# Kernel optimization log

Hardware: AMD Instinct MI355X
Metric: run time of the kernel (lower is better)

## Reference

```python
import jax, jax.numpy as jnp
import numpy as np

B, S, H = 2, 2048, 1024
NH, HD = 16, 64
EPS = 1e-12
SCALE = float(np.sqrt(HD))


def layer_norm(x, g, b, eps=EPS):
    m = jnp.mean(x, axis=-1, keepdims=True)
    v = jnp.mean(jnp.square(x - m), axis=-1, keepdims=True)
    return (x - m) * jax.lax.rsqrt(v + eps) * g + b


def setup_inputs() -> dict:
    key = jax.random.key(0)
    ks = jax.random.split(key, 12)
    std = 0.02 / np.sqrt(2 * 24)  # num_hidden_layers = 24
    return {
        "hidden_states": jax.random.normal(ks[0], (B, S, H), dtype=jnp.float32),
        "attention_mask": jnp.ones((B, S), dtype=jnp.float32),
        "Wq": jax.random.normal(ks[1], (H, H), dtype=jnp.float32) * std,
        "bq": jnp.zeros((H,), dtype=jnp.float32),
        "Wk": jax.random.normal(ks[2], (H, H), dtype=jnp.float32) * std,
        "bk": jnp.zeros((H,), dtype=jnp.float32),
        "Wv": jax.random.normal(ks[3], (H, H), dtype=jnp.float32) * std,
        "bv": jnp.zeros((H,), dtype=jnp.float32),
        "Wd": jax.random.normal(ks[4], (H, H), dtype=jnp.float32) * (1.0 / np.sqrt(H)),
        "bd": jnp.zeros((H,), dtype=jnp.float32),
        "ln_g": jnp.ones((H,), dtype=jnp.float32),
        "ln_b": jnp.zeros((H,), dtype=jnp.float32),
    }


def reference(hidden_states, attention_mask, Wq, bq, Wk, bk, Wv, bv, Wd, bd, ln_g, ln_b):
    x = hidden_states
    # NOTE: source computes pre_attention_norm(x) but the no-cache path uses raw x for Q/K/V.
    def heads(t):  # [B,S,H] -> [B,NH,S,HD]
        return t.reshape(B, S, NH, HD).transpose(0, 2, 1, 3)

    q = heads(x @ Wq.T + bq)
    k = heads(x @ Wk.T + bk)
    v = heads(x @ Wv.T + bv)

    scores = jnp.einsum("bhqd,bhkd->bhqk", q, k) / SCALE
    mask = (1.0 - attention_mask) * -10000.0  # [B,S] -> broadcast [B,1,1,S]
    scores = scores + mask[:, None, None, :]
    probs = jax.nn.softmax(scores.astype(jnp.float32), axis=-1).astype(x.dtype)

    ctx = jnp.einsum("bhqk,bhkd->bhqd", probs, v)
    ctx = ctx.transpose(0, 2, 1, 3).reshape(B, S, NH * HD)

    out = ctx @ Wd.T + bd
    out = layer_norm(out + x, ln_g, ln_b)
    out = jnp.where(jnp.isfinite(out), out, jnp.zeros_like(out))
    return out
```

## Files before the change

kernel.cpp:

```cpp
#include <hip/hip_runtime.h>
#include <cstdint>
#include <cstddef>

#define B_    2
#define S_    2048
#define H_    1024
#define NH_   16
#define HD_   64

typedef __attribute__((ext_vector_type(8)))  __bf16 bf16x8;
typedef __attribute__((ext_vector_type(4)))  __bf16 bf16x4;
typedef __attribute__((ext_vector_type(4)))  float  f32x4;
typedef __attribute__((ext_vector_type(16))) float  f32x16;
typedef __attribute__((ext_vector_type(4)))  unsigned u32x4;

typedef __attribute__((address_space(1))) const unsigned int gcu32_t;
typedef __attribute__((address_space(3))) unsigned int lu32_t;
#define GLOAD16(gp, lp) __builtin_amdgcn_global_load_lds((gcu32_t*)(gp), (lu32_t*)(lp), 16, 0, 0)

#if __has_builtin(__builtin_amdgcn_exp2f)
#define EXP2F(x) __builtin_amdgcn_exp2f(x)
#else
#define EXP2F(x) exp2f(x)
#endif

#define SC_Q 0.1803368977f

__device__ __forceinline__ short f2bf(float f) {
  union { float f; unsigned u; } v; v.f = f;
  unsigned r = v.u + 0x7fffu + ((v.u >> 16) & 1u);
  return (short)(r >> 16);
}

__global__ __launch_bounds__(256) void convert_kernel(
    const float* __restrict__ x,  const float* __restrict__ wq,
    const float* __restrict__ wk, const float* __restrict__ wv,
    const float* __restrict__ wd,
    short* __restrict__ xb,  short* __restrict__ wqb, short* __restrict__ wkb,
    short* __restrict__ wvb, short* __restrict__ wdb) {
  size_t i = ((size_t)blockIdx.x * 256 + threadIdx.x) * 4;
  const float* src; short* dst; size_t off;
  if      (i < 4194304u) { src = x;  dst = xb;  off = i; }
  else if (i < 5242880u) { src = wq; dst = wqb; off = i - 4194304u; }
  else if (i < 6291456u) { src = wk; dst = wkb; off = i - 5242880u; }
  else if (i < 7340032u) { src = wv; dst = wvb; off = i - 6291456u; }
  else                   { src = wd; dst = wdb; off = i - 7340032u; }
  float4 v = *(const float4*)(src + off);
  short4 o; o.x = f2bf(v.x); o.y = f2bf(v.y); o.z = f2bf(v.z); o.w = f2bf(v.w);
  *(short4*)(dst + off) = o;
}

template<int MODE>
__global__ __launch_bounds__(256, 3) void gemm_bt(
    const short* __restrict__ A,
    const short* __restrict__ Bq, const short* __restrict__ Bk,
    const short* __restrict__ Bv,
    const float* __restrict__ biasq, const float* __restrict__ biask,
    const float* __restrict__ biasv,
    short* __restrict__ outq, short* __restrict__ outk, short* __restrict__ outv,
    float* __restrict__ outy) {
  __shared__ short As[128 * 64];
  __shared__ short Bs[128 * 64];

  const short* Bw; const float* bias; short* outs = nullptr;
  float qscale = 1.0f;
  if (MODE == 0) {
    int z = blockIdx.z;
    Bw   = (z == 0) ? Bq    : ((z == 1) ? Bk    : Bv);
    bias = (z == 0) ? biasq : ((z == 1) ? biask : biasv);
    outs = (z == 0) ? outq  : ((z == 1) ? outk  : outv);
    if (z == 0) qscale = SC_Q;
  } else {
    Bw = Bq; bias = biasq;
  }

  const int K = 1024;
  int tid  = threadIdx.x;
  int lane = tid & 63, w = tid >> 6;
  int wr = w >> 1, wc = w & 1;
  int m0 = blockIdx.y * 128, n0 = blockIdx.x * 128;
  int l15 = lane & 15, lg = lane >> 4;

  int lr = lane >> 3, lc8 = 8 * ((lane & 7) ^ lr);
  const short* Ag = A  + (size_t)(m0 + w * 8 + lr) * K + lc8;
  const short* Bg = Bw + (size_t)(n0 + w * 8 + lr) * K + lc8;

  int cxor = (l15 & 7) * 8;

  f32x4 acc[4][4];
  for (int m = 0; m < 4; m++)
    for (int n = 0; n < 4; n++) acc[m][n] = {0.f, 0.f, 0.f, 0.f};

  for (int kt = 0; kt < 16; kt++) {
    __syncthreads();
    for (int it = 0; it < 4; it++) {
      GLOAD16(Ag + (size_t)it * 32 * K + kt * 64, &As[(w * 8 + it * 32) * 64]);
      GLOAD16(Bg + (size_t)it * 32 * K + kt * 64, &Bs[(w * 8 + it * 32) * 64]);
    }
    __syncthreads();
#pragma unroll
    for (int kkh = 0; kkh < 2; kkh++) {
      int col = (kkh * 32 + lg * 8) ^ cxor;
      bf16x8 af[4], bfr[4];
#pragma unroll
      for (int m = 0; m < 4; m++)
        af[m] = *(const bf16x8*)&As[(wr * 64 + m * 16 + l15) * 64 + col];
#pragma unroll
      for (int n = 0; n < 4; n++)
        bfr[n] = *(const bf16x8*)&Bs[(wc * 64 + n * 16 + l15) * 64 + col];
#pragma unroll
      for (int m = 0; m < 4; m++)
#pragma unroll
        for (int n = 0; n < 4; n++)
          acc[m][n] = __builtin_amdgcn_mfma_f32_16x16x32_bf16(af[m], bfr[n], acc[m][n], 0, 0, 0);
    }
  }

  for (int n = 0; n < 4; n++) {
    int col = n0 + wc * 64 + n * 16 + l15;
    float bval = bias[col];
    if (MODE == 0) {
      int h = col >> 6, d = col & 63;
      for (int m = 0; m < 4; m++) {
        int rowb = m0 + wr * 64 + m * 16 + lg * 4;
        for (int j = 0; j < 4; j++) {
          int row = rowb + j;
          int bb = row >> 11, s = row & 2047;
          outs[(((size_t)bb * NH_ + h) * S_ + s) * HD_ + d] = f2bf((acc[m][n][j] + bval) * qscale);
        }
      }
    } else {
      for (int m = 0; m < 4; m++) {
        int rowb = m0 + wr * 64 + m * 16 + lg * 4;
        for (int j = 0; j < 4; j++)
          outy[(size_t)(rowb + j) * 1024 + col] = acc[m][n][j] + bval;
      }
    }
  }
}

__global__ __launch_bounds__(256, 2) void attn_kernel(
    const short* __restrict__ Q, const short* __restrict__ K,
    const short* __restrict__ V, const float* __restrict__ mask,
    short* __restrict__ ctx) {
  __shared__ short Ks[2][64 * 64];
  __shared__ short Vs[2][64 * 64];
  __shared__ unsigned long long mbits[32];

  int b = blockIdx.x;
  int bh = (b & 7) * 4 + ((b >> 3) >> 4);
  int qb = (b >> 3) & 15;
  int bidx = bh >> 4, hh = bh & 15;
  int q0 = qb * 128;
  int tid = threadIdx.x, lane = tid & 63, w = tid >> 6;
  int l31 = lane & 31, lh = lane >> 5, l15 = lane & 15;

  const short* Qg = Q + (size_t)bh * S_ * HD_;
  const short* Kg = K + (size_t)bh * S_ * HD_;
  const short* Vg = V + (size_t)bh * S_ * HD_;

  int lr = lane >> 3, lc8 = 8 * ((lane & 7) ^ lr);
  int kxor = (lane & 7) * 8;

  const short* Qrow = Qg + (size_t)(q0 + w * 32 + l31) * HD_;
  bf16x8 qfrag[4];
#pragma unroll
  for (int ks = 0; ks < 4; ks++)
    qfrag[ks] = *(const bf16x8*)&Qrow[ks * 16 + lh * 8];

  GLOAD16(Kg + (size_t)(w * 8 + lr) * HD_ + lc8, &Ks[0][(w * 8) * 64]);
  GLOAD16(Kg + (size_t)(w * 8 + 32 + lr) * HD_ + lc8, &Ks[0][(w * 8 + 32) * 64]);
  int vrow = tid >> 3, vcol = (tid & 7) * 8;
  int voff = ((vrow >> 2) * 4 + (vcol >> 4)) * 64 + (vrow & 3) * 16 + (vcol & 15);
  *(int4*)&Vs[0][voff]        = *(const int4*)&Vg[(size_t)vrow * HD_ + vcol];
  *(int4*)&Vs[0][voff + 2048] = *(const int4*)&Vg[(size_t)(vrow + 32) * HD_ + vcol];
  if (w == 0) {
#pragma unroll 4
    for (int t = 0; t < 32; t++) {
      unsigned long long bb = __ballot(mask[bidx * S_ + t * 64 + lane] > 0.5f);
      if (lane == 0) mbits[t] = bb;
    }
  }
  __syncthreads();

  float mrun = -1e30f, lrun = 0.f;
  f32x16 oacc[2];
#pragma unroll
  for (int dt = 0; dt < 2; dt++)
#pragma unroll
    for (int j = 0; j < 16; j++) oacc[dt][j] = 0.f;

  unsigned vtrb = (unsigned)(uintptr_t)&Vs[0][0]
                + (unsigned)(l15 * 8 + ((lane >> 4) & 1) * 128 + lh * 1024);

  for (int kt = 0; kt < 32; kt++) {
    int cur = kt & 1;

    int4 vp0, vp1;
    if (kt < 31) {
      const short* Kn = Kg + (size_t)(kt + 1) * 64 * HD_;
      GLOAD16(Kn + (size_t)(w * 8 + lr) * HD_ + lc8, &Ks[cur ^ 1][(w * 8) * 64]);
      GLOAD16(Kn + (size_t)(w * 8 + 32 + lr) * HD_ + lc8, &Ks[cur ^ 1][(w * 8 + 32) * 64]);
      const short* Vn = Vg + (size_t)(kt + 1) * 64 * HD_;
      vp0 = *(const int4*)&Vn[(size_t)vrow * HD_ + vcol];
      vp1 = *(const int4*)&Vn[(size_t)(vrow + 32) * HD_ + vcol];
    }

    f32x16 sc[2];
#pragma unroll
    for (int kb = 0; kb < 2; kb++)
#pragma unroll
      for (int j = 0; j < 16; j++) sc[kb][j] = 0.f;
    __builtin_amdgcn_s_setprio(1);
#pragma unroll
    for (int ks = 0; ks < 4; ks++)
#pragma unroll
      for (int kb = 0; kb < 2; kb++) {
        bf16x8 af = *(const bf16x8*)&Ks[cur][(kb * 32 + l31) * 64 + ((ks * 16 + lh * 8) ^ kxor)];
        sc[kb] = __builtin_amdgcn_mfma_f32_32x32x16_bf16(af, qfrag[ks], sc[kb], 0, 0, 0);
      }
    __builtin_amdgcn_s_setprio(0);

    unsigned long long mb = mbits[kt];
    if (__any(mb != ~0ull)) {
      unsigned long long sh = mb >> (lh * 4);
#pragma unroll
      for (int kb = 0; kb < 2; kb++)
#pragma unroll
        for (int r = 0; r < 16; r++)
          if (!((sh >> (kb * 32 + (r & 3) + 8 * (r >> 2))) & 1)) sc[kb][r] = -1e30f;
    }

    float rmax = sc[0][0];
#pragma unroll
    for (int kb = 0; kb < 2; kb++)
#pragma unroll
      for (int r = 0; r < 16; r++) rmax = fmaxf(rmax, sc[kb][r]);
    {
      float xa = rmax, xb = rmax;
      asm volatile("v_permlane32_swap_b32 %0, %1" : "+v"(xa), "+v"(xb));
      rmax = fmaxf(xa, xb);
    }

    if (__any(rmax > mrun + 8.f)) {
      float mn = fmaxf(mrun, rmax);
      float a = EXP2F(mrun - mn);
      lrun *= a; mrun = mn;
#pragma unroll
      for (int dt = 0; dt < 2; dt++)
#pragma unroll
        for (int j = 0; j < 16; j++) oacc[dt][j] *= a;
    }

    float rs_ = 0.f;
#pragma unroll
    for (int kb = 0; kb < 2; kb++)
#pragma unroll
      for (int r = 0; r < 16; r++) {
        float p = EXP2F(sc[kb][r] - mrun);
        sc[kb][r] = p;
        rs_ += p;
      }
    {
      float xa = rs_, xb = rs_;
      asm volatile("v_permlane32_swap_b32 %0, %1" : "+v"(xa), "+v"(xb));
      rs_ = xa + xb;
    }
    lrun += rs_;

    bf16x8 pfrag[4];
#pragma unroll
    for (int ks = 0; ks < 4; ks++) {
      int kb = ks >> 1, ro = (ks & 1) * 8;
      unsigned X0, X1, X2, X3;
      asm("v_cvt_pk_bf16_f32 %0, %1, %2" : "=v"(X0) : "v"(sc[kb][ro + 0]), "v"(sc[kb][ro + 1]));
      asm("v_cvt_pk_bf16_f32 %0, %1, %2" : "=v"(X1) : "v"(sc[kb][ro + 2]), "v"(sc[kb][ro + 3]));
      asm("v_cvt_pk_bf16_f32 %0, %1, %2" : "=v"(X2) : "v"(sc[kb][ro + 4]), "v"(sc[kb][ro + 5]));
      asm("v_cvt_pk_bf16_f32 %0, %1, %2" : "=v"(X3) : "v"(sc[kb][ro + 6]), "v"(sc[kb][ro + 7]));
      asm volatile("v_permlane32_swap_b32 %0, %1" : "+v"(X0), "+v"(X2));
      asm volatile("v_permlane32_swap_b32 %0, %1" : "+v"(X1), "+v"(X3));
      union { u32x4 u; bf16x8 b; } cvt;
      cvt.u[0] = X0; cvt.u[1] = X1; cvt.u[2] = X2; cvt.u[3] = X3;
      pfrag[ks] = cvt.b;
    }

#pragma unroll
    for (int dt = 0; dt < 2; dt++) {
      bf16x4 vlo[4], vhi[4];
#pragma unroll
      for (int ks = 0; ks < 4; ks++) {
        unsigned a = vtrb + (unsigned)(cur * 8192 + ks * 2048 + dt * 256);
        asm volatile("ds_read_b64_tr_b16 %0, %2\n\t"
                     "ds_read_b64_tr_b16 %1, %2 offset:512"
                     : "=&v"(vlo[ks]), "=&v"(vhi[ks]) : "v"(a));
      }
      asm volatile("s_waitcnt lgkmcnt(0)" ::: "memory");
      __builtin_amdgcn_sched_barrier(0);
      __builtin_amdgcn_s_setprio(1);
#pragma unroll
      for (int ks = 0; ks < 4; ks++) {
        bf16x8 vb = __builtin_shufflevector(vlo[ks], vhi[ks], 0, 1, 2, 3, 4, 5, 6, 7);
        oacc[dt] = __builtin_amdgcn_mfma_f32_32x32x16_bf16(vb, pfrag[ks], oacc[dt], 0, 0, 0);
      }
      __builtin_amdgcn_s_setprio(0);
    }

    if (kt < 31) {
      *(int4*)&Vs[cur ^ 1][voff]        = vp0;
      *(int4*)&Vs[cur ^ 1][voff + 2048] = vp1;
    }
    __syncthreads();
  }

  float inv = 1.0f / lrun;
  int q = q0 + w * 32 + l31;
  size_t base = ((size_t)(bidx * S_ + q)) * H_ + hh * HD_;
#pragma unroll
  for (int dt = 0; dt < 2; dt++)
#pragma unroll
    for (int rr = 0; rr < 4; rr++) {
      int d0 = dt * 32 + rr * 8 + lh * 4;
      short4 st;
      st.x = f2bf(oacc[dt][rr * 4 + 0] * inv);
      st.y = f2bf(oacc[dt][rr * 4 + 1] * inv);
      st.z = f2bf(oacc[dt][rr * 4 + 2] * inv);
      st.w = f2bf(oacc[dt][rr * 4 + 3] * inv);
      *(short4*)&ctx[base + d0] = st;
    }
}

__global__ __launch_bounds__(256) void ln_kernel(
    const float* __restrict__ y, const float* __restrict__ x,
    const float* __restrict__ g, const float* __restrict__ bta,
    float* __restrict__ out) {
  __shared__ float red[4];
  int row = blockIdx.x;
  int tid = threadIdx.x, lane = tid & 63, w = tid >> 6;
  size_t base = (size_t)row * 1024 + tid * 4;
  float4 yv = *(const float4*)(y + base);
  float4 xv = *(const float4*)(x + base);
  float v0 = yv.x + xv.x, v1 = yv.y + xv.y, v2 = yv.z + xv.z, v3 = yv.w + xv.w;

  float ssum = v0 + v1 + v2 + v3;
  for (int off = 1; off < 64; off <<= 1) ssum += __shfl_xor(ssum, off);
  if (lane == 0) red[w] = ssum;
  __syncthreads();
  float mean = (red[0] + red[1] + red[2] + red[3]) * (1.f / 1024.f);
  __syncthreads();

  float d0 = v0 - mean, d1 = v1 - mean, d2 = v2 - mean, d3 = v3 - mean;
  float sq = d0 * d0 + d1 * d1 + d2 * d2 + d3 * d3;
  for (int off = 1; off < 64; off <<= 1) sq += __shfl_xor(sq, off);
  if (lane == 0) red[w] = sq;
  __syncthreads();
  float var = (red[0] + red[1] + red[2] + red[3]) * (1.f / 1024.f);
  float rs = 1.0f / sqrtf(var + 1e-12f);

  int c = tid * 4;
  float4 gv = *(const float4*)(g + c);
  float4 bv = *(const float4*)(bta + c);
  float o0 = d0 * rs * gv.x + bv.x;
  float o1 = d1 * rs * gv.y + bv.y;
  float o2 = d2 * rs * gv.z + bv.z;
  float o3 = d3 * rs * gv.w + bv.w;
  float4 ov;
  ov.x = __builtin_isfinite(o0) ? o0 : 0.f;
  ov.y = __builtin_isfinite(o1) ? o1 : 0.f;
  ov.z = __builtin_isfinite(o2) ? o2 : 0.f;
  ov.w = __builtin_isfinite(o3) ? o3 : 0.f;
  *(float4*)(out + base) = ov;
}

extern "C" void kernel_launch(void* const* d_in, const int* in_sizes, int n_in,
                              void* d_out, int out_size, void* d_ws, size_t ws_size,
                              hipStream_t stream) {
  (void)in_sizes; (void)n_in; (void)out_size; (void)ws_size;
  const float* x    = (const float*)d_in[0];
  const float* mask = (const float*)d_in[1];
  const float* Wq   = (const float*)d_in[2];
  const float* bq   = (const float*)d_in[3];
  const float* Wk   = (const float*)d_in[4];
  const float* bk   = (const float*)d_in[5];
  const float* Wv   = (const float*)d_in[6];
  const float* bv   = (const float*)d_in[7];
  const float* Wd   = (const float*)d_in[8];
  const float* bd   = (const float*)d_in[9];
  const float* ln_g = (const float*)d_in[10];
  const float* ln_b = (const float*)d_in[11];
  float* out = (float*)d_out;

  char* ws = (char*)d_ws;
  short* xb   = (short*)(ws);
  short* wqb  = (short*)(ws + ( 8ull << 20));
  short* wkb  = (short*)(ws + (10ull << 20));
  short* wvb  = (short*)(ws + (12ull << 20));
  short* wdb  = (short*)(ws + (14ull << 20));
  short* qb   = (short*)(ws + (16ull << 20));
  short* kb   = (short*)(ws + (24ull << 20));
  short* vb   = (short*)(ws + (32ull << 20));
  short* ctxb = (short*)(ws + (40ull << 20));
  float* y    = (float*)(ws + (48ull << 20));

  convert_kernel<<<8192, 256, 0, stream>>>(x, Wq, Wk, Wv, Wd, xb, wqb, wkb, wvb, wdb);
  gemm_bt<0><<<dim3(8, 32, 3), 256, 0, stream>>>(xb, wqb, wkb, wvb, bq, bk, bv,
                                                 qb, kb, vb, nullptr);
  attn_kernel<<<512, 256, 0, stream>>>(qb, kb, vb, mask, ctxb);
  gemm_bt<1><<<dim3(8, 32, 1), 256, 0, stream>>>(ctxb, wdb, nullptr, nullptr, bd,
                                                 nullptr, nullptr, nullptr, nullptr,
                                                 nullptr, y);
  ln_kernel<<<4096, 256, 0, stream>>>(y, x, ln_g, ln_b, out);
}
```

Baseline: 218.8 us.

## Split-K output GEMM, halve attention block size, tree-reduce softmax stats

```diff
diff --git a/kernel.cpp b/kernel.cpp
--- a/kernel.cpp
+++ b/kernel.cpp
@@ -58,12 +58,15 @@
     const float* __restrict__ biasq, const float* __restrict__ biask,
     const float* __restrict__ biasv,
     short* __restrict__ outq, short* __restrict__ outk, short* __restrict__ outv,
-    float* __restrict__ outy) {
+    float* __restrict__ outy, float* __restrict__ outy1) {
   __shared__ short As[128 * 64];
   __shared__ short Bs[128 * 64];
 
-  const short* Bw; const float* bias; short* outs = nullptr;
+  const short* Bw; const float* bias = nullptr; short* outs = nullptr;
+  float* youts = nullptr;
   float qscale = 1.0f;
+  const int KT = (MODE == 0) ? 16 : 8;
+  int koff = 0;
   if (MODE == 0) {
     int z = blockIdx.z;
     Bw   = (z == 0) ? Bq    : ((z == 1) ? Bk    : Bv);
@@ -71,7 +74,9 @@
     outs = (z == 0) ? outq  : ((z == 1) ? outk  : outv);
     if (z == 0) qscale = SC_Q;
   } else {
-    Bw = Bq; bias = biasq;
+    Bw = Bq;
+    koff = blockIdx.z * 512;
+    youts = (blockIdx.z == 0) ? outy : outy1;
   }
 
   const int K = 1024;
@@ -82,8 +87,8 @@
   int l15 = lane & 15, lg = lane >> 4;
 
   int lr = lane >> 3, lc8 = 8 * ((lane & 7) ^ lr);
-  const short* Ag = A  + (size_t)(m0 + w * 8 + lr) * K + lc8;
-  const short* Bg = Bw + (size_t)(n0 + w * 8 + lr) * K + lc8;
+  const short* Ag = A  + (size_t)(m0 + w * 8 + lr) * K + lc8 + koff;
+  const short* Bg = Bw + (size_t)(n0 + w * 8 + lr) * K + lc8 + koff;
 
   int cxor = (l15 & 7) * 8;
 
@@ -91,7 +96,7 @@
   for (int m = 0; m < 4; m++)
     for (int n = 0; n < 4; n++) acc[m][n] = {0.f, 0.f, 0.f, 0.f};
 
-  for (int kt = 0; kt < 16; kt++) {
+  for (int kt = 0; kt < KT; kt++) {
     __syncthreads();
     for (int it = 0; it < 4; it++) {
       GLOAD16(Ag + (size_t)it * 32 * K + kt * 64, &As[(w * 8 + it * 32) * 64]);
@@ -118,8 +123,8 @@
 
   for (int n = 0; n < 4; n++) {
     int col = n0 + wc * 64 + n * 16 + l15;
-    float bval = bias[col];
     if (MODE == 0) {
+      float bval = bias[col];
       int h = col >> 6, d = col & 63;
       for (int m = 0; m < 4; m++) {
         int rowb = m0 + wr * 64 + m * 16 + lg * 4;
@@ -133,13 +138,13 @@
       for (int m = 0; m < 4; m++) {
         int rowb = m0 + wr * 64 + m * 16 + lg * 4;
         for (int j = 0; j < 4; j++)
-          outy[(size_t)(rowb + j) * 1024 + col] = acc[m][n][j] + bval;
-      }
-    }
-  }
-}
-
-__global__ __launch_bounds__(256, 2) void attn_kernel(
+          youts[(size_t)(rowb + j) * 1024 + col] = acc[m][n][j];
+      }
+    }
+  }
+}
+
+__global__ __launch_bounds__(128, 2) void attn_kernel(
     const short* __restrict__ Q, const short* __restrict__ K,
     const short* __restrict__ V, const float* __restrict__ mask,
     short* __restrict__ ctx) {
@@ -148,10 +153,10 @@
   __shared__ unsigned long long mbits[32];
 
   int b = blockIdx.x;
-  int bh = (b & 7) * 4 + ((b >> 3) >> 4);
-  int qb = (b >> 3) & 15;
+  int bh = (b & 7) * 4 + ((b >> 3) >> 5);
+  int qb = (b >> 3) & 31;
   int bidx = bh >> 4, hh = bh & 15;
-  int q0 = qb * 128;
+  int q0 = qb * 64;
   int tid = threadIdx.x, lane = tid & 63, w = tid >> 6;
   int l31 = lane & 31, lh = lane >> 5, l15 = lane & 15;
 
@@ -168,18 +173,22 @@
   for (int ks = 0; ks < 4; ks++)
     qfrag[ks] = *(const bf16x8*)&Qrow[ks * 16 + lh * 8];
 
-  GLOAD16(Kg + (size_t)(w * 8 + lr) * HD_ + lc8, &Ks[0][(w * 8) * 64]);
-  GLOAD16(Kg + (size_t)(w * 8 + 32 + lr) * HD_ + lc8, &Ks[0][(w * 8 + 32) * 64]);
-  int vrow = tid >> 3, vcol = (tid & 7) * 8;
-  int voff = ((vrow >> 2) * 4 + (vcol >> 4)) * 64 + (vrow & 3) * 16 + (vcol & 15);
-  *(int4*)&Vs[0][voff]        = *(const int4*)&Vg[(size_t)vrow * HD_ + vcol];
-  *(int4*)&Vs[0][voff + 2048] = *(const int4*)&Vg[(size_t)(vrow + 32) * HD_ + vcol];
-  if (w == 0) {
-#pragma unroll 4
-    for (int t = 0; t < 32; t++) {
-      unsigned long long bb = __ballot(mask[bidx * S_ + t * 64 + lane] > 0.5f);
-      if (lane == 0) mbits[t] = bb;
-    }
+#pragma unroll
+  for (int it = 0; it < 4; it++) {
+    int r = w * 8 + it * 16;
+    GLOAD16(Kg + (size_t)(r + lr) * HD_ + lc8, &Ks[0][r * 64]);
+  }
+  int vrow = tid >> 1, vc0 = (tid & 1) * 32;
+  int voff[4];
+#pragma unroll
+  for (int c = 0; c < 4; c++) {
+    int vc = vc0 + c * 8;
+    voff[c] = ((vrow >> 2) * 4 + (vc >> 4)) * 64 + (vrow & 3) * 16 + (vc & 15);
+    *(int4*)&Vs[0][voff[c]] = *(const int4*)&Vg[(size_t)vrow * HD_ + vc];
+  }
+  for (int t = w; t < 32; t += 2) {
+    unsigned long long bb = __ballot(mask[bidx * S_ + t * 64 + lane] > 0.5f);
+    if (lane == 0) mbits[t] = bb;
   }
   __syncthreads();
 
@@ -196,14 +205,18 @@
   for (int kt = 0; kt < 32; kt++) {
     int cur = kt & 1;
 
-    int4 vp0, vp1;
+    int4 vp[4];
     if (kt < 31) {
       const short* Kn = Kg + (size_t)(kt + 1) * 64 * HD_;
-      GLOAD16(Kn + (size_t)(w * 8 + lr) * HD_ + lc8, &Ks[cur ^ 1][(w * 8) * 64]);
-      GLOAD16(Kn + (size_t)(w * 8 + 32 + lr) * HD_ + lc8, &Ks[cur ^ 1][(w * 8 + 32) * 64]);
+#pragma unroll
+      for (int it = 0; it < 4; it++) {
+        int r = w * 8 + it * 16;
+        GLOAD16(Kn + (size_t)(r + lr) * HD_ + lc8, &Ks[cur ^ 1][r * 64]);
+      }
       const short* Vn = Vg + (size_t)(kt + 1) * 64 * HD_;
-      vp0 = *(const int4*)&Vn[(size_t)vrow * HD_ + vcol];
-      vp1 = *(const int4*)&Vn[(size_t)(vrow + 32) * HD_ + vcol];
+#pragma unroll
+      for (int c = 0; c < 4; c++)
+        vp[c] = *(const int4*)&Vn[(size_t)vrow * HD_ + vc0 + c * 8];
     }
 
     f32x16 sc[2];
@@ -231,12 +244,17 @@
           if (!((sh >> (kb * 32 + (r & 3) + 8 * (r >> 2))) & 1)) sc[kb][r] = -1e30f;
     }
 
-    float rmax = sc[0][0];
-#pragma unroll
-    for (int kb = 0; kb < 2; kb++)
-#pragma unroll
-      for (int r = 0; r < 16; r++) rmax = fmaxf(rmax, sc[kb][r]);
+    float rmax;
     {
+      float t16[16], t8[8], t4[4], t2[2];
+#pragma unroll
+      for (int i = 0; i < 16; i++) t16[i] = fmaxf(sc[0][i], sc[1][i]);
+#pragma unroll
+      for (int i = 0; i < 8; i++) t8[i] = fmaxf(t16[i], t16[i + 8]);
+#pragma unroll
+      for (int i = 0; i < 4; i++) t4[i] = fmaxf(t8[i], t8[i + 4]);
+      t2[0] = fmaxf(t4[0], t4[2]); t2[1] = fmaxf(t4[1], t4[3]);
+      rmax = fmaxf(t2[0], t2[1]);
       float xa = rmax, xb = rmax;
       asm volatile("v_permlane32_swap_b32 %0, %1" : "+v"(xa), "+v"(xb));
       rmax = fmaxf(xa, xb);
@@ -252,16 +270,21 @@
         for (int j = 0; j < 16; j++) oacc[dt][j] *= a;
     }
 
-    float rs_ = 0.f;
 #pragma unroll
     for (int kb = 0; kb < 2; kb++)
 #pragma unroll
-      for (int r = 0; r < 16; r++) {
-        float p = EXP2F(sc[kb][r] - mrun);
-        sc[kb][r] = p;
-        rs_ += p;
-      }
+      for (int r = 0; r < 16; r++)
+        sc[kb][r] = EXP2F(sc[kb][r] - mrun);
+    float rs_;
     {
+      float s16[16], s8[8], s4[4];
+#pragma unroll
+      for (int i = 0; i < 16; i++) s16[i] = sc[0][i] + sc[1][i];
+#pragma unroll
+      for (int i = 0; i < 8; i++) s8[i] = s16[i] + s16[i + 8];
+#pragma unroll
+      for (int i = 0; i < 4; i++) s4[i] = s8[i] + s8[i + 4];
+      rs_ = (s4[0] + s4[1]) + (s4[2] + s4[3]);
       float xa = rs_, xb = rs_;
       asm volatile("v_permlane32_swap_b32 %0, %1" : "+v"(xa), "+v"(xb));
       rs_ = xa + xb;
@@ -306,8 +329,9 @@
     }
 
     if (kt < 31) {
-      *(int4*)&Vs[cur ^ 1][voff]        = vp0;
-      *(int4*)&Vs[cur ^ 1][voff + 2048] = vp1;
+#pragma unroll
+      for (int c = 0; c < 4; c++)
+        *(int4*)&Vs[cur ^ 1][voff[c]] = vp[c];
     }
     __syncthreads();
   }
@@ -330,16 +354,23 @@
 }
 
 __global__ __launch_bounds__(256) void ln_kernel(
-    const float* __restrict__ y, const float* __restrict__ x,
-    const float* __restrict__ g, const float* __restrict__ bta,
+    const float* __restrict__ y0p, const float* __restrict__ y1p,
+    const float* __restrict__ x,   const float* __restrict__ bd,
+    const float* __restrict__ g,   const float* __restrict__ bta,
     float* __restrict__ out) {
   __shared__ float red[4];
   int row = blockIdx.x;
   int tid = threadIdx.x, lane = tid & 63, w = tid >> 6;
   size_t base = (size_t)row * 1024 + tid * 4;
-  float4 yv = *(const float4*)(y + base);
-  float4 xv = *(const float4*)(x + base);
-  float v0 = yv.x + xv.x, v1 = yv.y + xv.y, v2 = yv.z + xv.z, v3 = yv.w + xv.w;
+  int c = tid * 4;
+  float4 y0v = *(const float4*)(y0p + base);
+  float4 y1v = *(const float4*)(y1p + base);
+  float4 xv  = *(const float4*)(x + base);
+  float4 bdv = *(const float4*)(bd + c);
+  float v0 = y0v.x + y1v.x + bdv.x + xv.x;
+  float v1 = y0v.y + y1v.y + bdv.y + xv.y;
+  float v2 = y0v.z + y1v.z + bdv.z + xv.z;
+  float v3 = y0v.w + y1v.w + bdv.w + xv.w;
 
   float ssum = v0 + v1 + v2 + v3;
   for (int off = 1; off < 64; off <<= 1) ssum += __shfl_xor(ssum, off);
@@ -356,7 +387,6 @@
   float var = (red[0] + red[1] + red[2] + red[3]) * (1.f / 1024.f);
   float rs = 1.0f / sqrtf(var + 1e-12f);
 
-  int c = tid * 4;
   float4 gv = *(const float4*)(g + c);
   float4 bv = *(const float4*)(bta + c);
   float o0 = d0 * rs * gv.x + bv.x;
@@ -399,14 +429,15 @@
   short* kb   = (short*)(ws + (24ull << 20));
   short* vb   = (short*)(ws + (32ull << 20));
   short* ctxb = (short*)(ws + (40ull << 20));
-  float* y    = (float*)(ws + (48ull << 20));
+  float* y0   = (float*)(ws + (48ull << 20));
+  float* y1   = (float*)(ws + (16ull << 20));
 
   convert_kernel<<<8192, 256, 0, stream>>>(x, Wq, Wk, Wv, Wd, xb, wqb, wkb, wvb, wdb);
   gemm_bt<0><<<dim3(8, 32, 3), 256, 0, stream>>>(xb, wqb, wkb, wvb, bq, bk, bv,
-                                                 qb, kb, vb, nullptr);
-  attn_kernel<<<512, 256, 0, stream>>>(qb, kb, vb, mask, ctxb);
-  gemm_bt<1><<<dim3(8, 32, 1), 256, 0, stream>>>(ctxb, wdb, nullptr, nullptr, bd,
+                                                 qb, kb, vb, nullptr, nullptr);
+  attn_kernel<<<1024, 128, 0, stream>>>(qb, kb, vb, mask, ctxb);
+  gemm_bt<1><<<dim3(8, 32, 2), 256, 0, stream>>>(ctxb, wdb, nullptr, nullptr, nullptr,
                                                  nullptr, nullptr, nullptr, nullptr,
-                                                 nullptr, y);
-  ln_kernel<<<4096, 256, 0, stream>>>(y, x, ln_g, ln_b, out);
-}
+                                                 nullptr, y0, y1);
+  ln_kernel<<<4096, 256, 0, stream>>>(y0, y1, x, bd, ln_g, ln_b, out);
+}
```

Measured after the change: 216.1 us. Within noise of the previous version (-1.2%).
